# Performance work log

Hardware: AMD Instinct MI355X
Metric: run time of the kernel (lower is better)

## Reference

```python
import jax, jax.numpy as jnp
import numpy as np

T, B, D, H = 512, 256, 256, 256


def setup_inputs() -> dict:
    key = jax.random.key(0)
    ks = jax.random.split(key, 10)
    # ragged lengths in [T//2, T], sorted descending as pack_padded_sequence requires
    lengths = np.sort(np.random.RandomState(0).randint(T // 2, T + 1, size=B))[::-1]
    # batch_sizes[t] = number of sequences still active at step t (non-increasing, >=1)
    batch_sizes = (lengths[None, :] > np.arange(T)[:, None]).sum(axis=1).astype(np.int32)
    batch_sizes = np.maximum(batch_sizes, 1)
    return {
        "input_x": jax.random.normal(ks[0], (T, B, D), jnp.float32),
        "h0": jax.random.normal(ks[1], (B, H), jnp.float32),
        "c0": jax.random.normal(ks[2], (B, H), jnp.float32),
        # variational dropout masks (precomputed, applied multiplicatively every step)
        "mask_x": (jax.random.uniform(ks[3], (B, D)) > 0.3).astype(jnp.float32) / 0.7,
        "mask_h": (jax.random.uniform(ks[4], (B, H)) > 0.3).astype(jnp.float32) / 0.7,
        "W_ih": jax.random.normal(ks[5], (4 * H, D), jnp.float32) * 0.05,
        "W_hh": jax.random.normal(ks[6], (4 * H, H), jnp.float32) * 0.05,
        "b_ih": jax.random.normal(ks[7], (4 * H,), jnp.float32) * 0.05,
        "b_hh": jax.random.normal(ks[8], (4 * H,), jnp.float32) * 0.05,
        "batch_sizes": jnp.asarray(batch_sizes),
    }


def reference(input_x, h0, c0, mask_x, mask_h, W_ih, W_hh, b_ih, b_hh, batch_sizes):
    # Forward (is_reversed=False) variational-dropout LSTM over a packed sequence.
    # Packed data is kept padded [T,B,*]; batch_sizes gives active rows per step.
    # Inactive rows keep their last-active hidden/cell state (== hn semantics).
    Bsz, Hid = h0.shape
    row = jnp.arange(Bsz)[:, None]

    def step(carry, inp):
        h, c = carry
        x_t, size = inp
        active = row < size  # [B,1]
        xi = x_t * mask_x            # input variational dropout
        hi = h * mask_h              # hidden variational dropout
        gates = xi @ W_ih.T + b_ih + hi @ W_hh.T + b_hh  # [B, 4H]
        i, f, g, o = jnp.split(gates, 4, axis=-1)
        c_new = jax.nn.sigmoid(f) * c + jax.nn.sigmoid(i) * jnp.tanh(g)
        h_new = jax.nn.sigmoid(o) * jnp.tanh(c_new)
        h = jnp.where(active, h_new, h)
        c = jnp.where(active, c_new, c)
        out = jnp.where(active, h_new, 0.0)  # padded positions zeroed (unused in pack)
        return (h, c), out

    (hn, cn), output = jax.lax.scan(step, (h0, c0), (input_x, batch_sizes))
    return output, hn, cn
```

## Files before the change

kernel.cpp:

```cpp
#include <hip/hip_runtime.h>
#include <hip/hip_bf16.h>

#define T_STEPS 512
#define BATCH   256
#define DIM     256
#define HID     256
#define DEPTH   4

using bf16x8  = __attribute__((ext_vector_type(8))) __bf16;
using floatx4 = __attribute__((ext_vector_type(4))) float;
typedef unsigned long long u64;
typedef unsigned int u32;

__device__ __forceinline__ float sigf(float x)   { return 1.0f / (1.0f + __expf(-x)); }
__device__ __forceinline__ float tanh_f(float x) { return 1.0f - 2.0f / (1.0f + __expf(2.0f * x)); }

__device__ __forceinline__ bf16x8 cvt8(const float* p) {
  floatx4 a = *(const floatx4*)p;
  floatx4 b = *(const floatx4*)(p + 4);
  bf16x8 r;
  r[0]=(__bf16)a[0]; r[1]=(__bf16)a[1]; r[2]=(__bf16)a[2]; r[3]=(__bf16)a[3];
  r[4]=(__bf16)b[0]; r[5]=(__bf16)b[1]; r[6]=(__bf16)b[2]; r[7]=(__bf16)b[3];
  return r;
}
__device__ __forceinline__ u32 f2bf(float f) {
  union { float f; u32 u; } v; v.f = f;
  u32 lsb = (v.u >> 16) & 1;
  return (v.u + 0x7fff + lsb) >> 16;
}
__device__ __forceinline__ float bf2f(u32 u) {
  union { u32 u; float f; } v; v.u = u << 16; return v.f;
}

__global__ void init_ws(int* __restrict__ flg, u64* __restrict__ inbox) {
  const int idx = blockIdx.x * 256 + threadIdx.x;
  if (idx < 4096) flg[idx] = 0;
  if (idx < 65536) inbox[idx] = 0ull;
}

__global__ __launch_bounds__(512, 1) void lstm_pk(
    const float* __restrict__ x, const float* __restrict__ h0,
    const float* __restrict__ c0,
    const float* __restrict__ mask_x, const float* __restrict__ mask_h,
    const float* __restrict__ W_ih, const float* __restrict__ W_hh,
    const float* __restrict__ b_ih, const float* __restrict__ b_hh,
    const int* __restrict__ bs_g,
    float* __restrict__ out, float* __restrict__ hn_out, float* __restrict__ cn_out,
    int* __restrict__ flg, float* __restrict__ ring, u64* __restrict__ inbox) {

  const int tid  = threadIdx.x;
  const int g    = blockIdx.x & 15;
  const int role = blockIdx.x >> 4;
  const int p    = role & 1;
  const int row_base = g * 16;
  const int lane = tid & 63;
  const int w    = tid >> 6;
  const int l15  = lane & 15;
  const int l4   = lane >> 4;

  __shared__ alignas(16) __bf16 s_ab[16 * 256];
  __shared__ int s_bs[T_STEPS];
  for (int i = tid; i < T_STEPS; i += 512) s_bs[i] = bs_g[i];
  __syncthreads();

  int* cons_flg_mine = flg + (g * 2 + p) * 32;
  int* prod_flg_mine = flg + 2048 + (g * 2 + p) * 32;
  float* ring_mine = ring + (size_t)(g * 2 + p) * (DEPTH * 8192);
  u64* inbox_mine    = inbox + (size_t)(g * 2 + p) * 2048;
  u64* inbox_partner = inbox + (size_t)(g * 2 + (1 - p)) * 2048;

  const int c_loc = w * 16 + l15;

  if (role >= 2) {
    bf16x8 wih_r[4][8];
    #pragma unroll
    for (int q = 0; q < 4; ++q) {
      const size_t wr = (size_t)(q * HID + p * 128 + c_loc) * DIM;
      #pragma unroll
      for (int m = 0; m < 8; ++m) wih_r[q][m] = cvt8(W_ih + wr + m * 32 + l4 * 8);
    }
    float bias[4];
    #pragma unroll
    for (int q = 0; q < 4; ++q) {
      const int bc = q * HID + p * 128 + c_loc;
      bias[q] = b_ih[bc] + b_hh[bc];
    }
    const int srow = tid & 15, scb = (tid >> 4) * 8;
    floatx4 mx0 = *(const floatx4*)(mask_x + (row_base + srow) * DIM + scb);
    floatx4 mx1 = *(const floatx4*)(mask_x + (row_base + srow) * DIM + scb + 4);
    const int soff = (srow * 512 + scb * 2) ^ ((srow & 7) << 4);

    for (int t = 0; t < T_STEPS; ++t) {
      if (s_bs[t] <= row_base) break;
      if (t >= DEPTH) {
        const int tgt = t - (DEPTH - 1);
        while (__hip_atomic_load(cons_flg_mine, __ATOMIC_RELAXED, __HIP_MEMORY_SCOPE_AGENT) < tgt) {}
      }
      const float* xp = x + ((size_t)t * BATCH + row_base + srow) * DIM + scb;
      floatx4 xa = *(const floatx4*)xp;
      floatx4 xb = *(const floatx4*)(xp + 4);
      bf16x8 xv;
      #pragma unroll
      for (int e = 0; e < 4; ++e) { xv[e] = (__bf16)(xa[e] * mx0[e]); xv[4 + e] = (__bf16)(xb[e] * mx1[e]); }
      *(bf16x8*)((char*)s_ab + soff) = xv;
      asm volatile("s_waitcnt lgkmcnt(0)" ::: "memory");
      __builtin_amdgcn_s_barrier();

      floatx4 a0, a1, a2, a3;
      a0 = a1 = a2 = a3 = (floatx4)(0.0f);
      #pragma unroll
      for (int m = 0; m < 8; ++m) {
        const int ab = (l15 * 512 + l4 * 16 + m * 64) ^ ((l15 & 7) << 4);
        bf16x8 ax = *(const bf16x8*)((const char*)s_ab + ab);
        a0 = __builtin_amdgcn_mfma_f32_16x16x32_bf16(ax, wih_r[0][m], a0, 0, 0, 0);
        a1 = __builtin_amdgcn_mfma_f32_16x16x32_bf16(ax, wih_r[1][m], a1, 0, 0, 0);
        a2 = __builtin_amdgcn_mfma_f32_16x16x32_bf16(ax, wih_r[2][m], a2, 0, 0, 0);
        a3 = __builtin_amdgcn_mfma_f32_16x16x32_bf16(ax, wih_r[3][m], a3, 0, 0, 0);
      }
      float* rs = ring_mine + (size_t)(t & (DEPTH - 1)) * 8192;
      #pragma unroll
      for (int e = 0; e < 4; ++e) {
        const int rb = (l4 * 4 + e) * 4;
        __hip_atomic_store(rs + (rb + 0) * 128 + c_loc, a0[e] + bias[0], __ATOMIC_RELAXED, __HIP_MEMORY_SCOPE_AGENT);
        __hip_atomic_store(rs + (rb + 1) * 128 + c_loc, a1[e] + bias[1], __ATOMIC_RELAXED, __HIP_MEMORY_SCOPE_AGENT);
        __hip_atomic_store(rs + (rb + 2) * 128 + c_loc, a2[e] + bias[2], __ATOMIC_RELAXED, __HIP_MEMORY_SCOPE_AGENT);
        __hip_atomic_store(rs + (rb + 3) * 128 + c_loc, a3[e] + bias[3], __ATOMIC_RELAXED, __HIP_MEMORY_SCOPE_AGENT);
      }
      asm volatile("s_waitcnt vmcnt(0)" ::: "memory");
      __builtin_amdgcn_s_barrier();
      if (tid == 0)
        __hip_atomic_store(prod_flg_mine, t + 1, __ATOMIC_RELAXED, __HIP_MEMORY_SCOPE_AGENT);
    }
    return;
  }

  const int c_own = p * 128 + c_loc;
  bf16x8 whh_r[4][8];
  #pragma unroll
  for (int q = 0; q < 4; ++q) {
    const size_t wr = (size_t)(q * HID + c_own) * HID;
    #pragma unroll
    for (int m = 0; m < 8; ++m) whh_r[q][m] = cvt8(W_hh + wr + m * 32 + l4 * 8);
  }
  float mh_c[4], h_[4], c_[4];
  #pragma unroll
  for (int e = 0; e < 4; ++e) {
    const int grow = row_base + l4 * 4 + e;
    mh_c[e] = mask_h[grow * HID + c_own];
    h_[e]   = h0[grow * HID + c_own];
    c_[e]   = c0[grow * HID + c_own];
  }
  const int sc_loc = tid >> 2;
  const int rq     = tid & 3;
  const int c_gs   = (1 - p) * 128 + sc_loc;
  float mh_s[4];
  #pragma unroll
  for (int e = 0; e < 4; ++e) mh_s[e] = mask_h[(row_base + rq * 4 + e) * HID + c_gs];

  while (__hip_atomic_load(prod_flg_mine, __ATOMIC_RELAXED, __HIP_MEMORY_SCOPE_AGENT) < 1) {}
  asm volatile("" ::: "memory");
  float xp_c[16];
  #pragma unroll
  for (int e = 0; e < 4; ++e)
    #pragma unroll
    for (int q = 0; q < 4; ++q)
      xp_c[e * 4 + q] = __hip_atomic_load(ring_mine + ((l4 * 4 + e) * 4 + q) * 128 + c_loc,
                                          __ATOMIC_RELAXED, __HIP_MEMORY_SCOPE_AGENT);

  for (int t = 0; t < T_STEPS; ++t) {
    const int bszt = s_bs[t];
    if (bszt <= row_base) {
      #pragma unroll
      for (int e = 0; e < 4; ++e)
        out[(size_t)t * (BATCH * HID) + (row_base + l4 * 4 + e) * HID + c_own] = 0.0f;
      continue;
    }
    const bool act_n = (t + 1 < T_STEPS) && (s_bs[t + 1] > row_base);

    #pragma unroll
    for (int e = 0; e < 4; ++e) {
      const int r = l4 * 4 + e;
      const int off = (r * 512 + c_own * 2) ^ ((r & 7) << 4);
      *(__bf16*)((char*)s_ab + off) = (__bf16)(h_[e] * mh_c[e]);
    }

    float xp_n[16];
    if (act_n) {
      while (__hip_atomic_load(prod_flg_mine, __ATOMIC_RELAXED, __HIP_MEMORY_SCOPE_AGENT) < t + 2) {}
      asm volatile("" ::: "memory");
      const float* rs = ring_mine + (size_t)((t + 1) & (DEPTH - 1)) * 8192;
      #pragma unroll
      for (int e = 0; e < 4; ++e)
        #pragma unroll
        for (int q = 0; q < 4; ++q)
          xp_n[e * 4 + q] = __hip_atomic_load(rs + ((l4 * 4 + e) * 4 + q) * 128 + c_loc,
                                              __ATOMIC_RELAXED, __HIP_MEMORY_SCOPE_AGENT);
    }

    if (t == 0) {
      #pragma unroll
      for (int e = 0; e < 4; ++e) {
        const int r = rq * 4 + e;
        const float hv = h0[(row_base + r) * HID + c_gs] * mh_s[e];
        const int off = (r * 512 + c_gs * 2) ^ ((r & 7) << 4);
        *(__bf16*)((char*)s_ab + off) = (__bf16)hv;
      }
    } else {
      const u64* ib = inbox_mine + (size_t)(t & 1) * 1024 + sc_loc * 8 + rq * 2;
      u64 pk0, pk1;
      do {
        pk0 = __hip_atomic_load(ib,     __ATOMIC_RELAXED, __HIP_MEMORY_SCOPE_AGENT);
        pk1 = __hip_atomic_load(ib + 1, __ATOMIC_RELAXED, __HIP_MEMORY_SCOPE_AGENT);
      } while (!__all(((u32)pk0 == (u32)t) && ((u32)pk1 == (u32)t)));
      float hv[4];
      hv[0] = bf2f((u32)(pk0 >> 32) & 0xffffu) * mh_s[0];
      hv[1] = bf2f((u32)(pk0 >> 48))           * mh_s[1];
      hv[2] = bf2f((u32)(pk1 >> 32) & 0xffffu) * mh_s[2];
      hv[3] = bf2f((u32)(pk1 >> 48))           * mh_s[3];
      #pragma unroll
      for (int e = 0; e < 4; ++e) {
        const int r = rq * 4 + e;
        const int off = (r * 512 + c_gs * 2) ^ ((r & 7) << 4);
        *(__bf16*)((char*)s_ab + off) = (__bf16)hv[e];
      }
    }

    asm volatile("s_waitcnt lgkmcnt(0)" ::: "memory");
    __builtin_amdgcn_s_barrier();

    floatx4 a0, a1, a2, a3;
    a0 = a1 = a2 = a3 = (floatx4)(0.0f);
    #pragma unroll
    for (int m = 0; m < 8; ++m) {
      const int ab = (l15 * 512 + l4 * 16 + m * 64) ^ ((l15 & 7) << 4);
      bf16x8 ah = *(const bf16x8*)((const char*)s_ab + ab);
      a0 = __builtin_amdgcn_mfma_f32_16x16x32_bf16(ah, whh_r[0][m], a0, 0, 0, 0);
      a1 = __builtin_amdgcn_mfma_f32_16x16x32_bf16(ah, whh_r[1][m], a1, 0, 0, 0);
      a2 = __builtin_amdgcn_mfma_f32_16x16x32_bf16(ah, whh_r[2][m], a2, 0, 0, 0);
      a3 = __builtin_amdgcn_mfma_f32_16x16x32_bf16(ah, whh_r[3][m], a3, 0, 0, 0);
    }

    float o_[4];
    #pragma unroll
    for (int e = 0; e < 4; ++e) {
      const bool ract = (row_base + l4 * 4 + e) < bszt;
      const float iv = sigf(a0[e] + xp_c[e * 4 + 0]);
      const float fv = sigf(a1[e] + xp_c[e * 4 + 1]);
      const float gv = tanh_f(a2[e] + xp_c[e * 4 + 2]);
      const float ov = sigf(a3[e] + xp_c[e * 4 + 3]);
      const float cc = fv * c_[e] + iv * gv;
      const float hh = ov * tanh_f(cc);
      if (ract) { c_[e] = cc; h_[e] = hh; }
      o_[e] = ract ? hh : 0.0f;
    }

    if (act_n) {
      u64* ob = inbox_partner + (size_t)((t + 1) & 1) * 1024 + c_loc * 8 + l4 * 2;
      const u64 tag = (u32)(t + 1);
      u64 w0 = tag | ((u64)f2bf(h_[0]) << 32) | ((u64)f2bf(h_[1]) << 48);
      u64 w1 = tag | ((u64)f2bf(h_[2]) << 32) | ((u64)f2bf(h_[3]) << 48);
      __hip_atomic_store(ob,     w0, __ATOMIC_RELAXED, __HIP_MEMORY_SCOPE_AGENT);
      __hip_atomic_store(ob + 1, w1, __ATOMIC_RELAXED, __HIP_MEMORY_SCOPE_AGENT);
      if (tid == 0)
        __hip_atomic_store(cons_flg_mine, t + 1, __ATOMIC_RELAXED, __HIP_MEMORY_SCOPE_AGENT);
    }

    #pragma unroll
    for (int e = 0; e < 4; ++e)
      out[(size_t)t * (BATCH * HID) + (row_base + l4 * 4 + e) * HID + c_own] = o_[e];

    __builtin_amdgcn_s_barrier();

    if (act_n) {
      #pragma unroll
      for (int i = 0; i < 16; ++i) xp_c[i] = xp_n[i];
    }
  }

  #pragma unroll
  for (int e = 0; e < 4; ++e) {
    const int grow = row_base + l4 * 4 + e;
    hn_out[grow * HID + c_own] = h_[e];
    cn_out[grow * HID + c_own] = c_[e];
  }
}

extern "C" void kernel_launch(void* const* d_in, const int* in_sizes, int n_in,
                              void* d_out, int out_size, void* d_ws, size_t ws_size,
                              hipStream_t stream) {
  const float* x      = (const float*)d_in[0];
  const float* h0     = (const float*)d_in[1];
  const float* c0     = (const float*)d_in[2];
  const float* mask_x = (const float*)d_in[3];
  const float* mask_h = (const float*)d_in[4];
  const float* W_ih   = (const float*)d_in[5];
  const float* W_hh   = (const float*)d_in[6];
  const float* b_ih   = (const float*)d_in[7];
  const float* b_hh   = (const float*)d_in[8];
  const int*   bs     = (const int*)d_in[9];

  float* out = (float*)d_out;
  float* hn  = out + (size_t)T_STEPS * BATCH * HID;
  float* cn  = hn + (size_t)BATCH * HID;

  int* flg  = (int*)d_ws;
  float* ring = (float*)((char*)d_ws + 16384);
  u64* inbox = (u64*)((char*)d_ws + 16384 + 4194304);

  init_ws<<<256, 256, 0, stream>>>(flg, inbox);
  lstm_pk<<<64, 512, 0, stream>>>(x, h0, c0, mask_x, mask_h, W_ih, W_hh,
                                  b_ih, b_hh, bs, out, hn, cn, flg, ring, inbox);
}
```

Before: 1.935 ms.

## Split recurrent MFMA so own-half runs before waiting on partner hidden state

Each block of the pair now writes its own masked h into LDS at the end of the previous step. It computes the K-half of the recurrent matmul that uses its own columns before polling the partner's inbox, then does the partner half after the exchange arrives. This overlaps half of the MFMA work with the cross-block latency on the critical path. The next-step projected-input prefetch moves after the output store, which removes the double-buffered xp_n registers but places that ring wait at the end of each step.

Result: slower. 4.803 ms (+148.2%).

```diff
diff --git a/kernel.cpp b/kernel.cpp
--- a/kernel.cpp
+++ b/kernel.cpp
@@ -38,7 +38,7 @@
   if (idx < 65536) inbox[idx] = 0ull;
 }
 
-__global__ __launch_bounds__(512, 1) void lstm_pk(
+__global__ __launch_bounds__(512, 1) void lstm_pk2(
     const float* __restrict__ x, const float* __restrict__ h0,
     const float* __restrict__ c0,
     const float* __restrict__ mask_x, const float* __restrict__ mask_h,
@@ -157,6 +157,15 @@
   #pragma unroll
   for (int e = 0; e < 4; ++e) mh_s[e] = mask_h[(row_base + rq * 4 + e) * HID + c_gs];
 
+  const int mo = p * 4;
+  const int mp = (1 - p) * 4;
+
+  #pragma unroll
+  for (int e = 0; e < 4; ++e) {
+    const int r = l4 * 4 + e;
+    const int off = (r * 512 + c_own * 2) ^ ((r & 7) << 4);
+    *(__bf16*)((char*)s_ab + off) = (__bf16)(h_[e] * mh_c[e]);
+  }
   while (__hip_atomic_load(prod_flg_mine, __ATOMIC_RELAXED, __HIP_MEMORY_SCOPE_AGENT) < 1) {}
   asm volatile("" ::: "memory");
   float xp_c[16];
@@ -166,6 +175,8 @@
     for (int q = 0; q < 4; ++q)
       xp_c[e * 4 + q] = __hip_atomic_load(ring_mine + ((l4 * 4 + e) * 4 + q) * 128 + c_loc,
                                           __ATOMIC_RELAXED, __HIP_MEMORY_SCOPE_AGENT);
+  asm volatile("s_waitcnt lgkmcnt(0)" ::: "memory");
+  __builtin_amdgcn_s_barrier();
 
   for (int t = 0; t < T_STEPS; ++t) {
     const int bszt = s_bs[t];
@@ -177,24 +188,17 @@
     }
     const bool act_n = (t + 1 < T_STEPS) && (s_bs[t + 1] > row_base);
 
-    #pragma unroll
-    for (int e = 0; e < 4; ++e) {
-      const int r = l4 * 4 + e;
-      const int off = (r * 512 + c_own * 2) ^ ((r & 7) << 4);
-      *(__bf16*)((char*)s_ab + off) = (__bf16)(h_[e] * mh_c[e]);
-    }
-
-    float xp_n[16];
-    if (act_n) {
-      while (__hip_atomic_load(prod_flg_mine, __ATOMIC_RELAXED, __HIP_MEMORY_SCOPE_AGENT) < t + 2) {}
-      asm volatile("" ::: "memory");
-      const float* rs = ring_mine + (size_t)((t + 1) & (DEPTH - 1)) * 8192;
-      #pragma unroll
-      for (int e = 0; e < 4; ++e)
-        #pragma unroll
-        for (int q = 0; q < 4; ++q)
-          xp_n[e * 4 + q] = __hip_atomic_load(rs + ((l4 * 4 + e) * 4 + q) * 128 + c_loc,
-                                              __ATOMIC_RELAXED, __HIP_MEMORY_SCOPE_AGENT);
+    floatx4 a0, a1, a2, a3;
+    a0 = a1 = a2 = a3 = (floatx4)(0.0f);
+    #pragma unroll
+    for (int i = 0; i < 4; ++i) {
+      const int m = mo + i;
+      const int ab = (l15 * 512 + l4 * 16 + m * 64) ^ ((l15 & 7) << 4);
+      bf16x8 ah = *(const bf16x8*)((const char*)s_ab + ab);
+      a0 = __builtin_amdgcn_mfma_f32_16x16x32_bf16(ah, whh_r[0][m], a0, 0, 0, 0);
+      a1 = __builtin_amdgcn_mfma_f32_16x16x32_bf16(ah, whh_r[1][m], a1, 0, 0, 0);
+      a2 = __builtin_amdgcn_mfma_f32_16x16x32_bf16(ah, whh_r[2][m], a2, 0, 0, 0);
+      a3 = __builtin_amdgcn_mfma_f32_16x16x32_bf16(ah, whh_r[3][m], a3, 0, 0, 0);
     }
 
     if (t == 0) {
@@ -211,7 +215,7 @@
       do {
         pk0 = __hip_atomic_load(ib,     __ATOMIC_RELAXED, __HIP_MEMORY_SCOPE_AGENT);
         pk1 = __hip_atomic_load(ib + 1, __ATOMIC_RELAXED, __HIP_MEMORY_SCOPE_AGENT);
-      } while (!__all(((u32)pk0 == (u32)t) && ((u32)pk1 == (u32)t)));
+      } while (!__all((int)(((u32)pk0 == (u32)t) && ((u32)pk1 == (u32)t))));
       float hv[4];
       hv[0] = bf2f((u32)(pk0 >> 32) & 0xffffu) * mh_s[0];
       hv[1] = bf2f((u32)(pk0 >> 48))           * mh_s[1];
@@ -224,14 +228,12 @@
         *(__bf16*)((char*)s_ab + off) = (__bf16)hv[e];
       }
     }
-
     asm volatile("s_waitcnt lgkmcnt(0)" ::: "memory");
     __builtin_amdgcn_s_barrier();
 
-    floatx4 a0, a1, a2, a3;
-    a0 = a1 = a2 = a3 = (floatx4)(0.0f);
-    #pragma unroll
-    for (int m = 0; m < 8; ++m) {
+    #pragma unroll
+    for (int i = 0; i < 4; ++i) {
+      const int m = mp + i;
       const int ab = (l15 * 512 + l4 * 16 + m * 64) ^ ((l15 & 7) << 4);
       bf16x8 ah = *(const bf16x8*)((const char*)s_ab + ab);
       a0 = __builtin_amdgcn_mfma_f32_16x16x32_bf16(ah, whh_r[0][m], a0, 0, 0, 0);
@@ -261,20 +263,36 @@
       u64 w1 = tag | ((u64)f2bf(h_[2]) << 32) | ((u64)f2bf(h_[3]) << 48);
       __hip_atomic_store(ob,     w0, __ATOMIC_RELAXED, __HIP_MEMORY_SCOPE_AGENT);
       __hip_atomic_store(ob + 1, w1, __ATOMIC_RELAXED, __HIP_MEMORY_SCOPE_AGENT);
+    }
+
+    if (act_n) {
+      #pragma unroll
+      for (int e = 0; e < 4; ++e) {
+        const int r = l4 * 4 + e;
+        const int off = (r * 512 + c_own * 2) ^ ((r & 7) << 4);
+        *(__bf16*)((char*)s_ab + off) = (__bf16)(h_[e] * mh_c[e]);
+      }
+    }
+    #pragma unroll
+    for (int e = 0; e < 4; ++e)
+      out[(size_t)t * (BATCH * HID) + (row_base + l4 * 4 + e) * HID + c_own] = o_[e];
+
+    if (act_n) {
       if (tid == 0)
         __hip_atomic_store(cons_flg_mine, t + 1, __ATOMIC_RELAXED, __HIP_MEMORY_SCOPE_AGENT);
-    }
-
-    #pragma unroll
-    for (int e = 0; e < 4; ++e)
-      out[(size_t)t * (BATCH * HID) + (row_base + l4 * 4 + e) * HID + c_own] = o_[e];
-
+      while (__hip_atomic_load(prod_flg_mine, __ATOMIC_RELAXED, __HIP_MEMORY_SCOPE_AGENT) < t + 2) {}
+      asm volatile("" ::: "memory");
+      const float* rs = ring_mine + (size_t)((t + 1) & (DEPTH - 1)) * 8192;
+      #pragma unroll
+      for (int e = 0; e < 4; ++e)
+        #pragma unroll
+        for (int q = 0; q < 4; ++q)
+          xp_c[e * 4 + q] = __hip_atomic_load(rs + ((l4 * 4 + e) * 4 + q) * 128 + c_loc,
+                                              __ATOMIC_RELAXED, __HIP_MEMORY_SCOPE_AGENT);
+    }
+
+    asm volatile("s_waitcnt lgkmcnt(0)" ::: "memory");
     __builtin_amdgcn_s_barrier();
-
-    if (act_n) {
-      #pragma unroll
-      for (int i = 0; i < 16; ++i) xp_c[i] = xp_n[i];
-    }
   }
 
   #pragma unroll
@@ -308,6 +326,6 @@
   u64* inbox = (u64*)((char*)d_ws + 16384 + 4194304);
 
   init_ws<<<256, 256, 0, stream>>>(flg, inbox);
-  lstm_pk<<<64, 512, 0, stream>>>(x, h0, c0, mask_x, mask_h, W_ih, W_hh,
-                                  b_ih, b_hh, bs, out, hn, cn, flg, ring, inbox);
-}
+  lstm_pk2<<<64, 512, 0, stream>>>(x, h0, c0, mask_x, mask_h, W_ih, W_hh,
+                                   b_ih, b_hh, bs, out, hn, cn, flg, ring, inbox);
+}
```
